# Kernel optimization log

Measured on AMD Instinct MI355X. Metric: run time of the kernel, lower is better.

Reference implementation:

```python
import jax, jax.numpy as jnp
import numpy as np

KH, KW = 2, 2  # kernel_shape: stride-2 zero-insertion unpool

def setup_inputs() -> dict:
    key = jax.random.key(0)
    x = jax.random.normal(key, (32, 112, 112, 64), dtype=jnp.float32)
    return {"x": x}

def reference(x) -> jnp.ndarray:
    # Equivalent to conv2d_transpose with identity-in-top-left kernel and
    # stride (KH, KW): each input element goes to the top-left of a KHxKW
    # zero block. Output shape: [B, H*KH, W*KW, C].
    b, h, w, c = x.shape
    out = jnp.zeros((b, h * KH, w * KW, c), dtype=x.dtype)
    out = out.at[:, ::KH, ::KW, :].set(x)
    return out
```

## Files before the change

### kernel.cpp

```cpp
#include <hip/hip_runtime.h>

typedef float f4 __attribute__((ext_vector_type(4)));

__global__ __launch_bounds__(256) void unpool_kernel(
    const f4* __restrict__ x, f4* __restrict__ out) {
    const int tid = threadIdx.x;
    const int j0  = blockIdx.x * 512 + tid;
    const int j1  = j0 + 256;
    const int h   = blockIdx.y;
    const int b   = blockIdx.z;

    const int c4_0 = j0 & 15, ow0 = j0 >> 4;
    const int c4_1 = j1 & 15, ow1 = j1 >> 4;

    const f4 z = (f4){0.f, 0.f, 0.f, 0.f};

    f4* orow_e = out + (size_t)(b * 224 + 2 * h) * 3584;
    f4* orow_o = orow_e + 3584;

    __builtin_nontemporal_store(z, &orow_o[j0]);
    __builtin_nontemporal_store(z, &orow_o[j1]);

    f4 v0 = z, v1 = z;
    if ((ow0 & 1) == 0) {
        const f4* xrow = x + (size_t)(b * 112 + h) * (112 * 16);
        v0 = __builtin_nontemporal_load(&xrow[(ow0 >> 1) * 16 + c4_0]);
        v1 = __builtin_nontemporal_load(&xrow[(ow1 >> 1) * 16 + c4_1]);
    }
    __builtin_nontemporal_store(v0, &orow_e[j0]);
    __builtin_nontemporal_store(v1, &orow_e[j1]);
}

extern "C" void kernel_launch(void* const* d_in, const int* in_sizes, int n_in,
                              void* d_out, int out_size, void* d_ws, size_t ws_size,
                              hipStream_t stream) {
    const f4* x = (const f4*)d_in[0];
    f4* out = (f4*)d_out;
    dim3 grid(7, 112, 32);
    dim3 block(256);
    unpool_kernel<<<grid, block, 0, stream>>>(x, out);
}
```

Before: 452.3 us.

## Split unpool into device memset plus sparse scatter of input values

Replaces the single kernel that wrote both zeros and values with a hipMemsetAsync that clears the whole output, followed by a scatter kernel that writes only the input elements to their even-position output slots. The aim is to use the runtime's fill path for the bulk zero writes and simplify the kernel. In exchange, the even-position output locations are written twice and a second operation is launched, which adds memory traffic.

Result: faster. 422.8 us (-6.5%).

```diff
diff --git a/kernel.cpp b/kernel.cpp
--- a/kernel.cpp
+++ b/kernel.cpp
@@ -2,41 +2,26 @@
 
 typedef float f4 __attribute__((ext_vector_type(4)));
 
-__global__ __launch_bounds__(256) void unpool_kernel(
+__global__ __launch_bounds__(256) void unpool_scatter(
     const f4* __restrict__ x, f4* __restrict__ out) {
-    const int tid = threadIdx.x;
-    const int j0  = blockIdx.x * 512 + tid;
-    const int j1  = j0 + 256;
-    const int h   = blockIdx.y;
-    const int b   = blockIdx.z;
+    const int j = blockIdx.x * 256 + threadIdx.x;
+    const int h = blockIdx.y;
+    const int b = blockIdx.z;
 
-    const int c4_0 = j0 & 15, ow0 = j0 >> 4;
-    const int c4_1 = j1 & 15, ow1 = j1 >> 4;
+    const f4* xrow = x + (size_t)(b * 112 + h) * 1792;
+    f4* orow = out + (size_t)(b * 224 + 2 * h) * 3584;
 
-    const f4 z = (f4){0.f, 0.f, 0.f, 0.f};
-
-    f4* orow_e = out + (size_t)(b * 224 + 2 * h) * 3584;
-    f4* orow_o = orow_e + 3584;
-
-    __builtin_nontemporal_store(z, &orow_o[j0]);
-    __builtin_nontemporal_store(z, &orow_o[j1]);
-
-    f4 v0 = z, v1 = z;
-    if ((ow0 & 1) == 0) {
-        const f4* xrow = x + (size_t)(b * 112 + h) * (112 * 16);
-        v0 = __builtin_nontemporal_load(&xrow[(ow0 >> 1) * 16 + c4_0]);
-        v1 = __builtin_nontemporal_load(&xrow[(ow1 >> 1) * 16 + c4_1]);
-    }
-    __builtin_nontemporal_store(v0, &orow_e[j0]);
-    __builtin_nontemporal_store(v1, &orow_e[j1]);
+    const f4 v = xrow[j];
+    const int o = ((j & ~15) << 1) | (j & 15);
+    __builtin_nontemporal_store(v, &orow[o]);
 }
 
 extern "C" void kernel_launch(void* const* d_in, const int* in_sizes, int n_in,
                               void* d_out, int out_size, void* d_ws, size_t ws_size,
                               hipStream_t stream) {
-    const f4* x = (const f4*)d_in[0];
-    f4* out = (f4*)d_out;
+    hipMemsetAsync(d_out, 0, (size_t)out_size, stream);
+
     dim3 grid(7, 112, 32);
     dim3 block(256);
-    unpool_kernel<<<grid, block, 0, stream>>>(x, out);
+    unpool_scatter<<<grid, block, 0, stream>>>((const f4*)d_in[0], (f4*)d_out);
 }
```
